# Kernel optimization log

Hardware: AMD Instinct MI355X
Metric: run time of the kernel (lower is better)

## Reference

```python
import jax, jax.numpy as jnp
import numpy as np

B, S, D, H, CLIP = 4, 1024, 1024, 16, 64
DH = D // H

def setup_inputs() -> dict:
    key = jax.random.key(0)
    ks = jax.random.split(key, 10)
    sc = 1.0 / np.sqrt(D)
    return {
        "queries": jax.random.normal(ks[0], (B, S, D), jnp.float32),
        "keys": jax.random.normal(ks[1], (B, S, D), jnp.float32),
        "values": jax.random.normal(ks[2], (B, S, D), jnp.float32),
        "valid_lens": jax.random.randint(ks[3], (B,), 0, S),
        "Wq": jax.random.normal(ks[4], (D, D), jnp.float32) * sc,
        "Wk": jax.random.normal(ks[5], (D, D), jnp.float32) * sc,
        "Wv": jax.random.normal(ks[6], (D, D), jnp.float32) * sc,
        "Wo": jax.random.normal(ks[7], (D, D), jnp.float32) * sc,
        "rpr_k": jax.random.normal(ks[8], (2 * CLIP + 1, DH), jnp.float32),
        "rpr_v": jax.random.normal(ks[9], (2 * CLIP + 1, DH), jnp.float32),
    }

def reference(queries, keys, values, valid_lens, Wq, Wk, Wv, Wo, rpr_k, rpr_v):
    # project and split heads: [B,S,D] -> [B,H,S,DH]
    def split(x, W):
        return (x @ W).reshape(B, S, H, DH).transpose(0, 2, 1, 3)
    q = split(queries, Wq)
    k = split(keys, Wk)
    v = split(values, Wv)
    # relative position indices [S,S] in [0, 2*CLIP]
    dist = jnp.arange(S)[None, :] - jnp.arange(S)[:, None]
    dist = jnp.clip(dist, -CLIP, CLIP) + CLIP
    pos_k = rpr_k[dist]  # [S,S,DH]
    pos_v = rpr_v[dist]  # [S,S,DH]
    # content scores + relative-position key bias
    scores = jnp.einsum('bhqd,bhkd->bhqk', q, k)
    scores = scores + jnp.einsum('bhqd,qkd->bhqk', q, pos_k)
    scores = scores / jnp.sqrt(jnp.asarray(DH, q.dtype))
    # masked softmax: positions >= valid_len set to -1e6 (matches torch code)
    key_mask = jnp.arange(S)[None, None, None, :] < valid_lens[:, None, None, None]
    scores = jnp.where(key_mask, scores, jnp.asarray(-1e6, scores.dtype))
    attn = jax.nn.softmax(scores, axis=-1)  # [B,H,S,S]
    # value aggregation + relative-position value bias
    out = jnp.einsum('bhqk,bhkd->bhqd', attn, v)
    out = out + jnp.einsum('bhqk,qkd->bhqd', attn, pos_v)
    out = out.transpose(0, 2, 1, 3).reshape(B, S, D)
    return out @ Wo
```

## Files before the change

kernel.cpp:

```cpp
#include <hip/hip_runtime.h>
#include <stdint.h>
#include <math.h>

#define BB 4
#define SS 1024
#define DD 1024
#define HH 16
#define DHH 64
#define NCLIP 64
#define NCC 129
#define NCP 160
#define QRSTR 148
#define M0F 20.0f

typedef __bf16 bf16;
typedef __bf16 bf16x8 __attribute__((ext_vector_type(8)));
typedef float f32x4 __attribute__((ext_vector_type(4)));

__device__ __forceinline__ void gload_lds16(const void* g, void* l) {
  __builtin_amdgcn_global_load_lds((const __attribute__((address_space(1))) void*)g,
                                   (__attribute__((address_space(3))) void*)l, 16, 0, 0);
}

struct TpArgs { const float* w[4]; bf16* wt[4]; };
__global__ __launch_bounds__(256) void transpose_pack_w(TpArgs args) {
  const float* __restrict__ W = args.w[blockIdx.z];
  bf16* __restrict__ Wt = args.wt[blockIdx.z];
  __shared__ float tile[32][33];
  int tx = threadIdx.x, ty = threadIdx.y;
  int n0 = blockIdx.x * 32, k0 = blockIdx.y * 32;
#pragma unroll
  for (int i = 0; i < 4; i++)
    tile[ty + i * 8][tx] = W[(size_t)(k0 + ty + i * 8) * DD + n0 + tx];
  __syncthreads();
#pragma unroll
  for (int i = 0; i < 4; i++)
    Wt[(size_t)(n0 + ty + i * 8) * DD + k0 + tx] = (bf16)tile[tx][ty + i * 8];
}

struct CvtArgs { const float* in[3]; bf16* out[3]; int skip[3]; };
__global__ __launch_bounds__(256) void f32_to_bf16_3(CvtArgs args, const int* __restrict__ vlens) {
  const int z = blockIdx.z;
  if (args.skip[z]) {
    int row0 = (blockIdx.x * 2) & 1023;
    int b = (blockIdx.x * 2) >> 10;
    int vl = vlens[b];
    if (vl > 0 && row0 >= vl) return;
  }
  const float* __restrict__ in = args.in[z];
  bf16* __restrict__ out = args.out[z];
  size_t i = ((size_t)blockIdx.x * 256 + threadIdx.x) * 8;
  f32x4 v0 = *(const f32x4*)(in + i);
  f32x4 v1 = *(const f32x4*)(in + i + 4);
  bf16x8 o;
#pragma unroll
  for (int j = 0; j < 4; j++) { o[j] = (bf16)v0[j]; o[j + 4] = (bf16)v1[j]; }
  *(bf16x8*)(out + i) = o;
}

struct GemmArgs { const bf16* a[3]; const bf16* bt[3]; void* c[3]; float sc[3]; int skip[3]; };
template <bool SPLIT>
__global__ __launch_bounds__(256) void gemm128(GemmArgs args, const int* __restrict__ vlens) {
  const int z = blockIdx.z;
  const int m0 = blockIdx.y * 128, n0 = blockIdx.x * 128;
  if (args.skip[z]) {
    int vl = vlens[m0 >> 10];
    if (vl > 0 && (m0 & 1023) >= vl) return;
  }
  const bf16* __restrict__ A  = args.a[z];
  const bf16* __restrict__ Bt = args.bt[z];
  void* __restrict__ Cv = args.c[z];
  const float scale = args.sc[z];
  __shared__ __align__(16) bf16 As[128][32];
  __shared__ __align__(16) bf16 Bs[128][32];
  const int tid = threadIdx.x, lane = tid & 63, wv = tid >> 6;
  const int wr = wv >> 1, wc = wv & 1;
  const int l15 = lane & 15, l4 = lane >> 4;
  const int srow = lane >> 2, scol = (lane & 3) * 8;
  f32x4 z4 = {0.f, 0.f, 0.f, 0.f};
  f32x4 acc[4][4];
#pragma unroll
  for (int i = 0; i < 4; i++)
#pragma unroll
    for (int j = 0; j < 4; j++) acc[i][j] = z4;

  for (int k0 = 0; k0 < DD; k0 += 32) {
    gload_lds16(A  + (size_t)(m0 + wv * 16 + srow) * DD + k0 + scol,      &As[wv * 16][0]);
    gload_lds16(A  + (size_t)(m0 + 64 + wv * 16 + srow) * DD + k0 + scol, &As[64 + wv * 16][0]);
    gload_lds16(Bt + (size_t)(n0 + wv * 16 + srow) * DD + k0 + scol,      &Bs[wv * 16][0]);
    gload_lds16(Bt + (size_t)(n0 + 64 + wv * 16 + srow) * DD + k0 + scol, &Bs[64 + wv * 16][0]);
    __syncthreads();
    bf16x8 af[4], bfv[4];
#pragma unroll
    for (int i = 0; i < 4; i++) {
      af[i]  = *(const bf16x8*)&As[wr * 64 + i * 16 + l15][l4 * 8];
      bfv[i] = *(const bf16x8*)&Bs[wc * 64 + i * 16 + l15][l4 * 8];
    }
#pragma unroll
    for (int mi = 0; mi < 4; mi++)
#pragma unroll
      for (int ni = 0; ni < 4; ni++)
        acc[mi][ni] = __builtin_amdgcn_mfma_f32_16x16x32_bf16(af[mi], bfv[ni], acc[mi][ni], 0, 0, 0);
    __syncthreads();
  }
#pragma unroll
  for (int mi = 0; mi < 4; mi++)
#pragma unroll
    for (int ni = 0; ni < 4; ni++)
#pragma unroll
      for (int r = 0; r < 4; r++) {
        int m = m0 + wr * 64 + mi * 16 + l4 * 4 + r;
        int n = n0 + wc * 64 + ni * 16 + l15;
        float val = acc[mi][ni][r] * scale;
        if (SPLIT) {
          ((bf16*)Cv)[((((size_t)(m >> 10) * HH + (n >> 6)) * SS) + (m & 1023)) * DHH + (n & 63)] =
              (bf16)val;
        } else {
          ((float*)Cv)[(size_t)m * DD + n] = val;
        }
      }
}

__global__ __launch_bounds__(256) void gemm_bf16_final(const bf16* __restrict__ A,
                                                       const bf16* __restrict__ Bt,
                                                       float* __restrict__ C) {
  __shared__ __align__(16) bf16 As[64][32];
  __shared__ __align__(16) bf16 Bs[128][32];
  const int tid = threadIdx.x, lane = tid & 63, wv = tid >> 6;
  const int l15 = lane & 15, l4 = lane >> 4;
  const int m0 = blockIdx.y * 64, n0 = blockIdx.x * 128;
  const int srow = lane >> 2, scol = (lane & 3) * 8;
  f32x4 z4 = {0.f, 0.f, 0.f, 0.f};
  f32x4 acc[4][2];
#pragma unroll
  for (int i = 0; i < 4; i++) { acc[i][0] = z4; acc[i][1] = z4; }

  for (int k0 = 0; k0 < DD; k0 += 32) {
    gload_lds16(A + (size_t)(m0 + wv * 16 + srow) * DD + k0 + scol, &As[wv * 16][0]);
    gload_lds16(Bt + (size_t)(n0 + wv * 32 + srow) * DD + k0 + scol, &Bs[wv * 32][0]);
    gload_lds16(Bt + (size_t)(n0 + wv * 32 + 16 + srow) * DD + k0 + scol, &Bs[wv * 32 + 16][0]);
    __syncthreads();
    bf16x8 af[4], bfv[2];
#pragma unroll
    for (int i = 0; i < 4; i++) af[i] = *(const bf16x8*)&As[i * 16 + l15][l4 * 8];
#pragma unroll
    for (int i = 0; i < 2; i++) bfv[i] = *(const bf16x8*)&Bs[wv * 32 + i * 16 + l15][l4 * 8];
#pragma unroll
    for (int mi = 0; mi < 4; mi++)
#pragma unroll
      for (int ni = 0; ni < 2; ni++)
        acc[mi][ni] = __builtin_amdgcn_mfma_f32_16x16x32_bf16(af[mi], bfv[ni], acc[mi][ni], 0, 0, 0);
    __syncthreads();
  }
#pragma unroll
  for (int mi = 0; mi < 4; mi++)
#pragma unroll
    for (int ni = 0; ni < 2; ni++)
#pragma unroll
      for (int r = 0; r < 4; r++) {
        int m = m0 + mi * 16 + l4 * 4 + r;
        int n = n0 + wv * 32 + ni * 16 + l15;
        C[(size_t)m * DD + n] = acc[mi][ni][r];
      }
}

__global__ __launch_bounds__(256) void vh_transpose(const bf16* __restrict__ Vh,
                                                    bf16* __restrict__ VhT,
                                                    const int* __restrict__ vlens) {
  __shared__ bf16 til[64][65];
  int bh = blockIdx.y;
  int s0 = blockIdx.x * 64;
  int vl = vlens[bh >> 4];
  if (vl > 0 && s0 >= vl + 32) return;
  const bf16* src = Vh + (size_t)bh * SS * DHH + (size_t)s0 * DHH;
  for (int i = threadIdx.x; i < 64 * 64; i += 256) {
    int r = i >> 6, cc = i & 63;
    til[r][cc] = src[(size_t)r * DHH + cc];
  }
  __syncthreads();
  bf16* dst = VhT + (size_t)bh * DHH * SS + s0;
  for (int i = threadIdx.x; i < 64 * 64; i += 256) {
    int d = i >> 6, cc = i & 63;
    dst[(size_t)d * SS + cc] = til[cc][d];
  }
}

__global__ void prep_tables(const float* __restrict__ rpr_v, const float* __restrict__ rpr_k,
                            bf16* __restrict__ rvT, bf16* __restrict__ rkP) {
  int i = blockIdx.x * 256 + threadIdx.x;
  if (i < DHH * NCP) {
    int d = i / NCP, c = i - d * NCP;
    rvT[i] = (c < NCC) ? (bf16)rpr_v[(size_t)c * DHH + d] : (bf16)0.f;
  }
  if (i < 144 * 64) {
    rkP[i] = (i < NCC * DHH) ? (bf16)rpr_k[i] : (bf16)0.f;
  }
}

__global__ __launch_bounds__(256, 3) void attn_mfma(
    const bf16* __restrict__ Qh, const bf16* __restrict__ Kh, const bf16* __restrict__ VhT,
    const bf16* __restrict__ rkP, const int* __restrict__ valid_lens,
    const bf16* __restrict__ rvT, bf16* __restrict__ Obh) {
  __shared__ __align__(16) bf16 Ks[32][64];
  __shared__ __align__(16) bf16 Vs[64][32];
  __shared__ __align__(16) char arena[4][10240];
  const int tid = threadIdx.x, lane = tid & 63, w = tid >> 6;
  const int l15 = lane & 15, l4 = lane >> 4;
  const int b = blockIdx.z, h = blockIdx.y, bh = b * HH + h;
  const int q0 = blockIdx.x * 64 + w * 16;
  const int vlen = valid_lens[b];
  const float mval = (vlen == 0) ? 0.f : -30000.f;
  char* base = arena[w];
  bf16* QRs = (bf16*)base;
  _Float16* SBand = (_Float16*)(base + 4736);
  bf16* Pl = (bf16*)(base + 8832);

  const bf16* Qbase = Qh + ((size_t)bh * SS + q0) * DHH;
  bf16x8 qa0 = *(const bf16x8*)(Qbase + (size_t)l15 * DHH + l4 * 8);
  bf16x8 qa1 = *(const bf16x8*)(Qbase + (size_t)l15 * DHH + 32 + l4 * 8);
  const bf16* Kbase = Kh + (size_t)bh * SS * DHH;
  const bf16* Vbase = VhT + (size_t)bh * DHH * SS;
  f32x4 z = {0.f, 0.f, 0.f, 0.f};

#pragma unroll
  for (int ni = 0; ni < 9; ni++) {
    const bf16* rp = rkP + (size_t)(ni * 16 + l15) * DHH + l4 * 8;
    bf16x8 b0 = *(const bf16x8*)(rp);
    bf16x8 b1 = *(const bf16x8*)(rp + 32);
    f32x4 acc = __builtin_amdgcn_mfma_f32_16x16x32_bf16(qa0, b0, z, 0, 0, 0);
    acc = __builtin_amdgcn_mfma_f32_16x16x32_bf16(qa1, b1, acc, 0, 0, 0);
#pragma unroll
    for (int r = 0; r < 4; r++)
      QRs[(l4 * 4 + r) * QRSTR + ni * 16 + l15] = (bf16)acc[r];
  }
  {
    _Float16 ninf = (_Float16)(-65504.f);
    for (int i = lane; i < 16 * 128; i += 64) SBand[i] = ninf;
  }

  float biasLo[4], biasHi[4];
#pragma unroll
  for (int r = 0; r < 4; r++) {
    biasLo[r] = (float)QRs[(l4 * 4 + r) * QRSTR + 0];
    biasHi[r] = (float)QRs[(l4 * 4 + r) * QRSTR + 128];
  }

  float l_lane[4], slo[4], shi[4];
#pragma unroll
  for (int r = 0; r < 4; r++) { l_lane[r] = 0.f; slo[r] = 0.f; shi[r] = 0.f; }
  f32x4 acco[4];
#pragma unroll
  for (int i = 0; i < 4; i++) acco[i] = z;

  const int ksw0 = (l4 ^ (l15 & 7)) * 8;
  const int ksw1 = ((l4 + 4) ^ (l15 & 7)) * 8;
  const int vsw  = (l4 ^ (l15 & 3)) * 8;
  const int krow = w * 8 + (lane >> 3);
  const int kch  = ((lane & 7) ^ (krow & 7)) * 8;
  const int vd   = w * 16 + (lane >> 2);
  const int vch  = ((lane & 3) ^ (vd & 3)) * 8;

  const int kfb = (vlen > 0) ? (vlen & ~31) : 0;
  const int kte = (vlen > 0) ? ((vlen + 31) & ~31) : SS;
  int bs = q0 - 94; bs = (bs < 0) ? 0 : ((bs + 31) & ~31);
  int be = (q0 + 110) & ~31; if (be > SS) be = SS;

  for (int ks = 0; ks < kte; ks += 32) {
    gload_lds16(Kbase + (size_t)(ks + krow) * DHH + kch, &Ks[w * 8][0]);
    gload_lds16(Vbase + (size_t)vd * SS + ks + vch, &Vs[w * 16][0]);
    __syncthreads();
    bf16x8 kf00 = *(const bf16x8*)&Ks[l15][ksw0];
    bf16x8 kf01 = *(const bf16x8*)&Ks[l15][ksw1];
    bf16x8 kf10 = *(const bf16x8*)&Ks[16 + l15][ksw0];
    bf16x8 kf11 = *(const bf16x8*)&Ks[16 + l15][ksw1];
    f32x4 a0 = __builtin_amdgcn_mfma_f32_16x16x32_bf16(qa0, kf00, z, 0, 0, 0);
    a0 = __builtin_amdgcn_mfma_f32_16x16x32_bf16(qa1, kf01, a0, 0, 0, 0);
    f32x4 a1 = __builtin_amdgcn_mfma_f32_16x16x32_bf16(qa0, kf10, z, 0, 0, 0);
    a1 = __builtin_amdgcn_mfma_f32_16x16x32_bf16(qa1, kf11, a1, 0, 0, 0);

    if (ks >= kfb) {
      const int rel = ks - q0;
      const int mode = (rel <= -95) ? 0 : (rel >= 79) ? 1 : 2;
#pragma unroll
      for (int sub = 0; sub < 2; sub++) {
        const f32x4 a = sub ? a1 : a0;
        const int kg = ks + sub * 16 + l15;
        const bool msk = (kg >= vlen);
        if (mode == 0) {
#pragma unroll
          for (int r = 0; r < 4; r++) {
            float s = msk ? mval : (a[r] + biasLo[r]);
            float p = __expf(s - M0F);
            l_lane[r] += p; slo[r] += p;
            Pl[(l4 * 4 + r) * 40 + sub * 16 + l15] = (bf16)p;
          }
        } else if (mode == 1) {
#pragma unroll
          for (int r = 0; r < 4; r++) {
            float s = msk ? mval : (a[r] + biasHi[r]);
            float p = __expf(s - M0F);
            l_lane[r] += p; shi[r] += p;
            Pl[(l4 * 4 + r) * 40 + sub * 16 + l15] = (bf16)p;
          }
        } else {
#pragma unroll
          for (int r = 0; r < 4; r++) {
            const int qloc = l4 * 4 + r;
            int dlt = kg - q0 - qloc;
            int c = (dlt < -NCLIP ? -NCLIP : (dlt > NCLIP ? NCLIP : dlt)) + NCLIP;
            float s = a[r] + (float)QRs[qloc * QRSTR + c];
            if (msk) s = mval;
            if (dlt > -64 && dlt < 64) SBand[qloc * 128 + dlt + 63] = (_Float16)s;
            float p = __expf(s - M0F);
            l_lane[r] += p;
            slo[r] += (dlt <= -64) ? p : 0.f;
            shi[r] += (dlt >= 64) ? p : 0.f;
            Pl[qloc * 40 + sub * 16 + l15] = (bf16)p;
          }
        }
      }
    } else if (ks < bs) {
#pragma unroll
      for (int sub = 0; sub < 2; sub++) {
        const f32x4 a = sub ? a1 : a0;
#pragma unroll
        for (int r = 0; r < 4; r++) {
          float p = __expf(a[r] + biasLo[r] - M0F);
          l_lane[r] += p; slo[r] += p;
          Pl[(l4 * 4 + r) * 40 + sub * 16 + l15] = (bf16)p;
        }
      }
    } else if (ks < be) {
#pragma unroll
      for (int sub = 0; sub < 2; sub++) {
        const f32x4 a = sub ? a1 : a0;
        const int kg = ks + sub * 16 + l15;
#pragma unroll
        for (int r = 0; r < 4; r++) {
          const int qloc = l4 * 4 + r;
          int dlt = kg - q0 - qloc;
          int c = (dlt < -NCLIP ? -NCLIP : (dlt > NCLIP ? NCLIP : dlt)) + NCLIP;
          float s = a[r] + (float)QRs[qloc * QRSTR + c];
          if (dlt > -64 && dlt < 64) SBand[qloc * 128 + dlt + 63] = (_Float16)s;
          float p = __expf(s - M0F);
          l_lane[r] += p;
          slo[r] += (dlt <= -64) ? p : 0.f;
          shi[r] += (dlt >= 64) ? p : 0.f;
          Pl[qloc * 40 + sub * 16 + l15] = (bf16)p;
        }
      }
    } else {
#pragma unroll
      for (int sub = 0; sub < 2; sub++) {
        const f32x4 a = sub ? a1 : a0;
#pragma unroll
        for (int r = 0; r < 4; r++) {
          float p = __expf(a[r] + biasHi[r] - M0F);
          l_lane[r] += p; shi[r] += p;
          Pl[(l4 * 4 + r) * 40 + sub * 16 + l15] = (bf16)p;
        }
      }
    }

    bf16x8 pa = *(const bf16x8*)&Pl[l15 * 40 + l4 * 8];
    acco[0] = __builtin_amdgcn_mfma_f32_16x16x32_bf16(pa, *(const bf16x8*)&Vs[l15][vsw], acco[0], 0, 0, 0);
    acco[1] = __builtin_amdgcn_mfma_f32_16x16x32_bf16(pa, *(const bf16x8*)&Vs[16 + l15][vsw], acco[1], 0, 0, 0);
    acco[2] = __builtin_amdgcn_mfma_f32_16x16x32_bf16(pa, *(const bf16x8*)&Vs[32 + l15][vsw], acco[2], 0, 0, 0);
    acco[3] = __builtin_amdgcn_mfma_f32_16x16x32_bf16(pa, *(const bf16x8*)&Vs[48 + l15][vsw], acco[3], 0, 0, 0);
    __syncthreads();
  }

  float* li_s   = (float*)(base + 8832);
  float* a0_s   = (float*)(base + 8896);
  float* a128_s = (float*)(base + 8960);
  float li_r[4];
#pragma unroll
  for (int r = 0; r < 4; r++) {
    const int qloc = l4 * 4 + r;
    float lt = l_lane[r], so = slo[r], sh = shi[r];
    lt += __shfl_xor(lt, 1, 64); so += __shfl_xor(so, 1, 64); sh += __shfl_xor(sh, 1, 64);
    lt += __shfl_xor(lt, 2, 64); so += __shfl_xor(so, 2, 64); sh += __shfl_xor(sh, 2, 64);
    lt += __shfl_xor(lt, 4, 64); so += __shfl_xor(so, 4, 64); sh += __shfl_xor(sh, 4, 64);
    lt += __shfl_xor(lt, 8, 64); so += __shfl_xor(so, 8, 64); sh += __shfl_xor(sh, 8, 64);
    float li = 1.f / lt;
    li_r[r] = li;
    if (l15 == 0) { li_s[qloc] = li; a0_s[qloc] = so * li; a128_s[qloc] = sh * li; }
  }
  bf16* AWs = (bf16*)base;
  for (int row = 0; row < 16; row++) {
    float li = li_s[row], a0 = a0_s[row], a128 = a128_s[row];
#pragma unroll
    for (int j = 0; j < 3; j++) {
      int c = lane + 64 * j;
      if (c < 160) {
        float val;
        if (c == 0) val = a0;
        else if (c == 128) val = a128;
        else if (c < 128) val = __expf((float)SBand[row * 128 + c - 1] - M0F) * li;
        else val = 0.f;
        AWs[row * 168 + c] = (bf16)val;
      }
    }
  }
  f32x4 acc2[4];
#pragma unroll
  for (int i = 0; i < 4; i++) acc2[i] = z;
#pragma unroll
  for (int kk = 0; kk < 5; kk++) {
    bf16x8 af = *(const bf16x8*)&AWs[l15 * 168 + kk * 32 + l4 * 8];
#pragma unroll
    for (int ni = 0; ni < 4; ni++) {
      bf16x8 bv = *(const bf16x8*)(rvT + (size_t)(ni * 16 + l15) * NCP + kk * 32 + l4 * 8);
      acc2[ni] = __builtin_amdgcn_mfma_f32_16x16x32_bf16(af, bv, acc2[ni], 0, 0, 0);
    }
  }
#pragma unroll
  for (int ni = 0; ni < 4; ni++)
#pragma unroll
    for (int r = 0; r < 4; r++) {
      int qg = q0 + l4 * 4 + r;
      Obh[((size_t)b * SS + qg) * DD + h * DHH + ni * 16 + l15] =
          (bf16)(acco[ni][r] * li_r[r] + acc2[ni][r]);
    }
}

extern "C" void kernel_launch(void* const* d_in, const int* in_sizes, int n_in,
                              void* d_out, int out_size, void* d_ws, size_t ws_size,
                              hipStream_t stream) {
  (void)in_sizes; (void)n_in; (void)out_size; (void)ws_size;
  const float* queries = (const float*)d_in[0];
  const float* keys    = (const float*)d_in[1];
  const float* values  = (const float*)d_in[2];
  const int*   vlens   = (const int*)d_in[3];
  const float* Wq = (const float*)d_in[4];
  const float* Wk = (const float*)d_in[5];
  const float* Wv = (const float*)d_in[6];
  const float* Wo = (const float*)d_in[7];
  const float* rpr_k = (const float*)d_in[8];
  const float* rpr_v = (const float*)d_in[9];

  char* ws = (char*)d_ws;
  const size_t MB = 1024 * 1024;
  bf16* Wtq  = (bf16*)(ws + 0 * MB);
  bf16* Wtk  = (bf16*)(ws + 2 * MB);
  bf16* Wtv  = (bf16*)(ws + 4 * MB);
  bf16* Wto  = (bf16*)(ws + 6 * MB);
  bf16* Qh   = (bf16*)(ws + 8 * MB);
  bf16* Kh   = (bf16*)(ws + 16 * MB);
  bf16* Vh   = (bf16*)(ws + 24 * MB);
  bf16* VhT  = (bf16*)(ws + 32 * MB);
  bf16* Qb   = (bf16*)(ws + 40 * MB);
  bf16* Kb   = (bf16*)(ws + 48 * MB);
  bf16* Vb   = (bf16*)(ws + 56 * MB);
  bf16* Obh  = (bf16*)(ws + 64 * MB);
  bf16* rvT  = (bf16*)(ws + 72 * MB);
  bf16* rkP  = (bf16*)(ws + 73 * MB);

  TpArgs tp; tp.w[0] = Wq; tp.w[1] = Wk; tp.w[2] = Wv; tp.w[3] = Wo;
  tp.wt[0] = Wtq; tp.wt[1] = Wtk; tp.wt[2] = Wtv; tp.wt[3] = Wto;
  transpose_pack_w<<<dim3(32, 32, 4), dim3(32, 8), 0, stream>>>(tp);

  CvtArgs cv; cv.in[0] = queries; cv.in[1] = keys; cv.in[2] = values;
  cv.out[0] = Qb; cv.out[1] = Kb; cv.out[2] = Vb;
  cv.skip[0] = 0; cv.skip[1] = 1; cv.skip[2] = 1;
  f32_to_bf16_3<<<dim3(2048, 1, 3), 256, 0, stream>>>(cv, vlens);

  GemmArgs gp;
  gp.a[0] = Qb; gp.a[1] = Kb; gp.a[2] = Vb;
  gp.bt[0] = Wtq; gp.bt[1] = Wtk; gp.bt[2] = Wtv;
  gp.c[0] = (void*)Qh; gp.c[1] = (void*)Kh; gp.c[2] = (void*)Vh;
  gp.sc[0] = 0.125f; gp.sc[1] = 1.0f; gp.sc[2] = 1.0f;
  gp.skip[0] = 0; gp.skip[1] = 1; gp.skip[2] = 1;
  gemm128<true><<<dim3(8, 32, 3), 256, 0, stream>>>(gp, vlens);

  vh_transpose<<<dim3(16, 64), 256, 0, stream>>>(Vh, VhT, vlens);
  prep_tables<<<dim3(40), 256, 0, stream>>>(rpr_v, rpr_k, rvT, rkP);
  attn_mfma<<<dim3(16, HH, BB), 256, 0, stream>>>(Qh, Kh, VhT, rkP, vlens, rvT, Obh);
  gemm_bf16_final<<<dim3(8, 64), 256, 0, stream>>>(Obh, Wto, (float*)d_out);
}
```

Baseline: 114.5 us.

## Fuse fp32-to-bf16 conversion into projection GEMM; double-buffer K and read V directly

```diff
diff --git a/kernel.cpp b/kernel.cpp
--- a/kernel.cpp
+++ b/kernel.cpp
@@ -38,28 +38,8 @@
     Wt[(size_t)(n0 + ty + i * 8) * DD + k0 + tx] = (bf16)tile[tx][ty + i * 8];
 }
 
-struct CvtArgs { const float* in[3]; bf16* out[3]; int skip[3]; };
-__global__ __launch_bounds__(256) void f32_to_bf16_3(CvtArgs args, const int* __restrict__ vlens) {
-  const int z = blockIdx.z;
-  if (args.skip[z]) {
-    int row0 = (blockIdx.x * 2) & 1023;
-    int b = (blockIdx.x * 2) >> 10;
-    int vl = vlens[b];
-    if (vl > 0 && row0 >= vl) return;
-  }
-  const float* __restrict__ in = args.in[z];
-  bf16* __restrict__ out = args.out[z];
-  size_t i = ((size_t)blockIdx.x * 256 + threadIdx.x) * 8;
-  f32x4 v0 = *(const f32x4*)(in + i);
-  f32x4 v1 = *(const f32x4*)(in + i + 4);
-  bf16x8 o;
-#pragma unroll
-  for (int j = 0; j < 4; j++) { o[j] = (bf16)v0[j]; o[j + 4] = (bf16)v1[j]; }
-  *(bf16x8*)(out + i) = o;
-}
-
-struct GemmArgs { const bf16* a[3]; const bf16* bt[3]; void* c[3]; float sc[3]; int skip[3]; };
-template <bool SPLIT>
+struct GemmArgs { const void* a[3]; const bf16* bt[3]; void* c[3]; float sc[3]; int skip[3]; };
+template <bool SPLIT, bool AF32>
 __global__ __launch_bounds__(256) void gemm128(GemmArgs args, const int* __restrict__ vlens) {
   const int z = blockIdx.z;
   const int m0 = blockIdx.y * 128, n0 = blockIdx.x * 128;
@@ -67,7 +47,6 @@
     int vl = vlens[m0 >> 10];
     if (vl > 0 && (m0 & 1023) >= vl) return;
   }
-  const bf16* __restrict__ A  = args.a[z];
   const bf16* __restrict__ Bt = args.bt[z];
   void* __restrict__ Cv = args.c[z];
   const float scale = args.sc[z];
@@ -77,6 +56,7 @@
   const int wr = wv >> 1, wc = wv & 1;
   const int l15 = lane & 15, l4 = lane >> 4;
   const int srow = lane >> 2, scol = (lane & 3) * 8;
+  const int arow = tid >> 1, akb = (tid & 1) * 16;
   f32x4 z4 = {0.f, 0.f, 0.f, 0.f};
   f32x4 acc[4][4];
 #pragma unroll
@@ -85,8 +65,26 @@
     for (int j = 0; j < 4; j++) acc[i][j] = z4;
 
   for (int k0 = 0; k0 < DD; k0 += 32) {
-    gload_lds16(A  + (size_t)(m0 + wv * 16 + srow) * DD + k0 + scol,      &As[wv * 16][0]);
-    gload_lds16(A  + (size_t)(m0 + 64 + wv * 16 + srow) * DD + k0 + scol, &As[64 + wv * 16][0]);
+    if (AF32) {
+      const float* Af = (const float*)args.a[z];
+      const float* src = Af + (size_t)(m0 + arow) * DD + k0 + akb;
+      f32x4 v0 = *(const f32x4*)(src + 0);
+      f32x4 v1 = *(const f32x4*)(src + 4);
+      f32x4 v2 = *(const f32x4*)(src + 8);
+      f32x4 v3 = *(const f32x4*)(src + 12);
+      bf16x8 o0, o1;
+#pragma unroll
+      for (int j = 0; j < 4; j++) {
+        o0[j] = (bf16)v0[j]; o0[j + 4] = (bf16)v1[j];
+        o1[j] = (bf16)v2[j]; o1[j + 4] = (bf16)v3[j];
+      }
+      *(bf16x8*)&As[arow][akb] = o0;
+      *(bf16x8*)&As[arow][akb + 8] = o1;
+    } else {
+      const bf16* Ab = (const bf16*)args.a[z];
+      gload_lds16(Ab + (size_t)(m0 + wv * 16 + srow) * DD + k0 + scol,      &As[wv * 16][0]);
+      gload_lds16(Ab + (size_t)(m0 + 64 + wv * 16 + srow) * DD + k0 + scol, &As[64 + wv * 16][0]);
+    }
     gload_lds16(Bt + (size_t)(n0 + wv * 16 + srow) * DD + k0 + scol,      &Bs[wv * 16][0]);
     gload_lds16(Bt + (size_t)(n0 + 64 + wv * 16 + srow) * DD + k0 + scol, &Bs[64 + wv * 16][0]);
     __syncthreads();
@@ -201,8 +199,7 @@
     const bf16* __restrict__ Qh, const bf16* __restrict__ Kh, const bf16* __restrict__ VhT,
     const bf16* __restrict__ rkP, const int* __restrict__ valid_lens,
     const bf16* __restrict__ rvT, bf16* __restrict__ Obh) {
-  __shared__ __align__(16) bf16 Ks[32][64];
-  __shared__ __align__(16) bf16 Vs[64][32];
+  __shared__ __align__(16) bf16 Ks[2][32][64];
   __shared__ __align__(16) char arena[4][10240];
   const int tid = threadIdx.x, lane = tid & 63, w = tid >> 6;
   const int l15 = lane & 15, l4 = lane >> 4;
@@ -252,27 +249,28 @@
 #pragma unroll
   for (int i = 0; i < 4; i++) acco[i] = z;
 
+  const int krow = w * 8 + (lane >> 3);
+  const int kch  = ((lane & 7) ^ (krow & 7)) * 8;
   const int ksw0 = (l4 ^ (l15 & 7)) * 8;
   const int ksw1 = ((l4 + 4) ^ (l15 & 7)) * 8;
-  const int vsw  = (l4 ^ (l15 & 3)) * 8;
-  const int krow = w * 8 + (lane >> 3);
-  const int kch  = ((lane & 7) ^ (krow & 7)) * 8;
-  const int vd   = w * 16 + (lane >> 2);
-  const int vch  = ((lane & 3) ^ (vd & 3)) * 8;
 
   const int kfb = (vlen > 0) ? (vlen & ~31) : 0;
   const int kte = (vlen > 0) ? ((vlen + 31) & ~31) : SS;
   int bs = q0 - 94; bs = (bs < 0) ? 0 : ((bs + 31) & ~31);
   int be = (q0 + 110) & ~31; if (be > SS) be = SS;
 
+  gload_lds16(Kbase + (size_t)krow * DHH + kch, &Ks[0][w * 8][0]);
+  __syncthreads();
+
+  int cur = 0;
   for (int ks = 0; ks < kte; ks += 32) {
-    gload_lds16(Kbase + (size_t)(ks + krow) * DHH + kch, &Ks[w * 8][0]);
-    gload_lds16(Vbase + (size_t)vd * SS + ks + vch, &Vs[w * 16][0]);
-    __syncthreads();
-    bf16x8 kf00 = *(const bf16x8*)&Ks[l15][ksw0];
-    bf16x8 kf01 = *(const bf16x8*)&Ks[l15][ksw1];
-    bf16x8 kf10 = *(const bf16x8*)&Ks[16 + l15][ksw0];
-    bf16x8 kf11 = *(const bf16x8*)&Ks[16 + l15][ksw1];
+    if (ks + 32 < kte)
+      gload_lds16(Kbase + (size_t)(ks + 32 + krow) * DHH + kch, &Ks[cur ^ 1][w * 8][0]);
+
+    bf16x8 kf00 = *(const bf16x8*)&Ks[cur][l15][ksw0];
+    bf16x8 kf01 = *(const bf16x8*)&Ks[cur][l15][ksw1];
+    bf16x8 kf10 = *(const bf16x8*)&Ks[cur][16 + l15][ksw0];
+    bf16x8 kf11 = *(const bf16x8*)&Ks[cur][16 + l15][ksw1];
     f32x4 a0 = __builtin_amdgcn_mfma_f32_16x16x32_bf16(qa0, kf00, z, 0, 0, 0);
     a0 = __builtin_amdgcn_mfma_f32_16x16x32_bf16(qa1, kf01, a0, 0, 0, 0);
     f32x4 a1 = __builtin_amdgcn_mfma_f32_16x16x32_bf16(qa0, kf10, z, 0, 0, 0);
@@ -363,11 +361,13 @@
     }
 
     bf16x8 pa = *(const bf16x8*)&Pl[l15 * 40 + l4 * 8];
-    acco[0] = __builtin_amdgcn_mfma_f32_16x16x32_bf16(pa, *(const bf16x8*)&Vs[l15][vsw], acco[0], 0, 0, 0);
-    acco[1] = __builtin_amdgcn_mfma_f32_16x16x32_bf16(pa, *(const bf16x8*)&Vs[16 + l15][vsw], acco[1], 0, 0, 0);
-    acco[2] = __builtin_amdgcn_mfma_f32_16x16x32_bf16(pa, *(const bf16x8*)&Vs[32 + l15][vsw], acco[2], 0, 0, 0);
-    acco[3] = __builtin_amdgcn_mfma_f32_16x16x32_bf16(pa, *(const bf16x8*)&Vs[48 + l15][vsw], acco[3], 0, 0, 0);
+    const bf16* vp = Vbase + (size_t)l15 * SS + ks + l4 * 8;
+    acco[0] = __builtin_amdgcn_mfma_f32_16x16x32_bf16(pa, *(const bf16x8*)(vp), acco[0], 0, 0, 0);
+    acco[1] = __builtin_amdgcn_mfma_f32_16x16x32_bf16(pa, *(const bf16x8*)(vp + (size_t)16 * SS), acco[1], 0, 0, 0);
+    acco[2] = __builtin_amdgcn_mfma_f32_16x16x32_bf16(pa, *(const bf16x8*)(vp + (size_t)32 * SS), acco[2], 0, 0, 0);
+    acco[3] = __builtin_amdgcn_mfma_f32_16x16x32_bf16(pa, *(const bf16x8*)(vp + (size_t)48 * SS), acco[3], 0, 0, 0);
     __syncthreads();
+    cur ^= 1;
   }
 
   float* li_s   = (float*)(base + 8832);
@@ -449,29 +449,21 @@
   bf16* Kh   = (bf16*)(ws + 16 * MB);
   bf16* Vh   = (bf16*)(ws + 24 * MB);
   bf16* VhT  = (bf16*)(ws + 32 * MB);
-  bf16* Qb   = (bf16*)(ws + 40 * MB);
-  bf16* Kb   = (bf16*)(ws + 48 * MB);
-  bf16* Vb   = (bf16*)(ws + 56 * MB);
-  bf16* Obh  = (bf16*)(ws + 64 * MB);
-  bf16* rvT  = (bf16*)(ws + 72 * MB);
-  bf16* rkP  = (bf16*)(ws + 73 * MB);
+  bf16* Obh  = (bf16*)(ws + 40 * MB);
+  bf16* rvT  = (bf16*)(ws + 48 * MB);
+  bf16* rkP  = (bf16*)(ws + 49 * MB);
 
   TpArgs tp; tp.w[0] = Wq; tp.w[1] = Wk; tp.w[2] = Wv; tp.w[3] = Wo;
   tp.wt[0] = Wtq; tp.wt[1] = Wtk; tp.wt[2] = Wtv; tp.wt[3] = Wto;
   transpose_pack_w<<<dim3(32, 32, 4), dim3(32, 8), 0, stream>>>(tp);
 
-  CvtArgs cv; cv.in[0] = queries; cv.in[1] = keys; cv.in[2] = values;
-  cv.out[0] = Qb; cv.out[1] = Kb; cv.out[2] = Vb;
-  cv.skip[0] = 0; cv.skip[1] = 1; cv.skip[2] = 1;
-  f32_to_bf16_3<<<dim3(2048, 1, 3), 256, 0, stream>>>(cv, vlens);
-
   GemmArgs gp;
-  gp.a[0] = Qb; gp.a[1] = Kb; gp.a[2] = Vb;
+  gp.a[0] = queries; gp.a[1] = keys; gp.a[2] = values;
   gp.bt[0] = Wtq; gp.bt[1] = Wtk; gp.bt[2] = Wtv;
   gp.c[0] = (void*)Qh; gp.c[1] = (void*)Kh; gp.c[2] = (void*)Vh;
   gp.sc[0] = 0.125f; gp.sc[1] = 1.0f; gp.sc[2] = 1.0f;
   gp.skip[0] = 0; gp.skip[1] = 1; gp.skip[2] = 1;
-  gemm128<true><<<dim3(8, 32, 3), 256, 0, stream>>>(gp, vlens);
+  gemm128<true, true><<<dim3(8, 32, 3), 256, 0, stream>>>(gp, vlens);
 
   vh_transpose<<<dim3(16, 64), 256, 0, stream>>>(Vh, VhT, vlens);
   prep_tables<<<dim3(40), 256, 0, stream>>>(rpr_v, rpr_k, rvT, rkP);
```

After: 134.4 us. 1.17x slower.
